# Kernel optimization log

Hardware: AMD Instinct MI355X
Metric: run time of the kernel (lower is better)

Reference implementation:

```python
import jax, jax.numpy as jnp
import numpy as np

N_GROUPS = 32
N_HEADS = 16
EPS = 1e-5


def group_norm(x, w, b):
    # x: [B, C, T]
    B, C, T = x.shape
    xg = x.reshape(B, N_GROUPS, C // N_GROUPS, T)
    mu = xg.mean(axis=(2, 3), keepdims=True)
    var = xg.var(axis=(2, 3), keepdims=True)
    xn = ((xg - mu) * jax.lax.rsqrt(var + EPS)).reshape(B, C, T)
    return xn * w[None, :, None] + b[None, :, None]


def setup_inputs() -> dict:
    key = jax.random.key(0)
    ks = jax.random.split(key, 5)
    B, C, T = 4, 1024, 1024
    return {
        "x": jax.random.normal(ks[0], (B, C, T), jnp.float32),
        "norm_weight": jnp.ones((C,), jnp.float32),
        "norm_bias": jnp.zeros((C,), jnp.float32),
        "qkv_w": jax.random.normal(ks[1], (3 * C, C), jnp.float32) * 0.02,
        "qkv_b": jax.random.normal(ks[2], (3 * C,), jnp.float32) * 0.02,
        "proj_w": jax.random.normal(ks[3], (C, C), jnp.float32) * 0.02,
        "proj_b": jax.random.normal(ks[4], (C,), jnp.float32) * 0.02,
    }


def reference(x, norm_weight, norm_bias, qkv_w, qkv_b, proj_w, proj_b):
    B, C, T = x.shape
    H = N_HEADS
    ch = C // H
    # GroupNorm + 1x1 conv to QKV: [B, 3C, T]
    xn = group_norm(x, norm_weight, norm_bias)
    qkv = jnp.einsum('oc,bct->bot', qkv_w, xn) + qkv_b[None, :, None]
    # Legacy layout: [B, H*3*ch, T] -> [B, H, 3, ch, T]
    qkv = qkv.reshape(B, H, 3, ch, T)
    q, k, v = qkv[:, :, 0], qkv[:, :, 1], qkv[:, :, 2]
    scale = 1.0 / jnp.sqrt(jnp.sqrt(jnp.asarray(ch, x.dtype)))
    w = jnp.einsum('bhct,bhcs->bhts', q * scale, k * scale)
    w = jax.nn.softmax(w.astype(jnp.float32), axis=-1).astype(w.dtype)
    a = jnp.einsum('bhts,bhcs->bhct', w, v).reshape(B, C, T)
    h = jnp.einsum('oc,bct->bot', proj_w, a) + proj_b[None, :, None]
    return x + h
```

## Files before the change

kernel.cpp:

```cpp
#include <hip/hip_runtime.h>
#include <hip/hip_bf16.h>

typedef __bf16 bf16;
typedef bf16  bf16x4 __attribute__((ext_vector_type(4)));
typedef bf16  bf16x8 __attribute__((ext_vector_type(8)));
typedef float f32x4  __attribute__((ext_vector_type(4)));

union B8 { bf16x8 v; bf16 e[8]; };
union B4 { bf16x4 v; bf16 e[4]; };
union F4 { f32x4 v; float e[4]; };

#define GLOAD_LDS16(g, l)                                            \
  __builtin_amdgcn_global_load_lds(                                  \
      (const __attribute__((address_space(1))) void*)(g),            \
      (__attribute__((address_space(3))) void*)(l), 16, 0, 0)

#define SWZ(arr, R, c8) (*(const bf16x8*)&(arr)[(size_t)(R) * 64 + (((c8) ^ ((R) & 7)) << 3)])

__global__ __launch_bounds__(256) void pre_kernel(
    const float* __restrict__ x, const float* __restrict__ w,
    const float* __restrict__ bias, bf16* __restrict__ xnt,
    const float* __restrict__ qkvw, const float* __restrict__ qkvb,
    const float* __restrict__ pw,
    bf16* __restrict__ Wb, bf16* __restrict__ Pb, float* __restrict__ bs)
{
  const int tid = threadIdx.x;

  if (blockIdx.x >= 128) {
    const int row = blockIdx.x - 128;
    if (row < 3072) {
      const float s = ((row % 192) < 128) ? 0.42468158f : 1.0f;
      const float4 a = ((const float4*)(qkvw + (size_t)row * 1024))[tid];
      B4 o;
      o.e[0] = (bf16)(a.x * s); o.e[1] = (bf16)(a.y * s);
      o.e[2] = (bf16)(a.z * s); o.e[3] = (bf16)(a.w * s);
      ((bf16x4*)(Wb + (size_t)row * 1024))[tid] = o.v;
      if (tid == 0) bs[row] = qkvb[row] * s;
    } else {
      const int r = row - 3072;
      const float4 a = ((const float4*)(pw + (size_t)r * 1024))[tid];
      B4 o;
      o.e[0] = (bf16)a.x; o.e[1] = (bf16)a.y;
      o.e[2] = (bf16)a.z; o.e[3] = (bf16)a.w;
      ((bf16x4*)(Pb + (size_t)r * 1024))[tid] = o.v;
    }
    return;
  }

  const int blk = blockIdx.x;
  const int b = blk >> 5, g = blk & 31;
  const float* xp = x + (size_t)(b * 1024 + g * 32) * 1024;

  float s = 0.f, ss = 0.f;
  for (int ch = tid; ch < 4096; ch += 256) {
    const float4* p = (const float4*)(xp + (size_t)ch * 8);
    float4 u0 = p[0], u1 = p[1];
    s  += u0.x + u0.y + u0.z + u0.w + u1.x + u1.y + u1.z + u1.w;
    ss += u0.x*u0.x + u0.y*u0.y + u0.z*u0.z + u0.w*u0.w
        + u1.x*u1.x + u1.y*u1.y + u1.z*u1.z + u1.w*u1.w;
  }
  #pragma unroll
  for (int m = 1; m < 64; m <<= 1) { s += __shfl_xor(s, m); ss += __shfl_xor(ss, m); }

  __shared__ float red[8];
  __shared__ float stats[2];
  const int wave = tid >> 6, lane = tid & 63;
  if (lane == 0) { red[wave] = s; red[4 + wave] = ss; }
  __syncthreads();
  if (tid == 0) {
    float ts  = red[0] + red[1] + red[2] + red[3];
    float tss = red[4] + red[5] + red[6] + red[7];
    float mu  = ts * (1.f / 32768.f);
    float var = tss * (1.f / 32768.f) - mu * mu;
    stats[0] = mu;
    stats[1] = rsqrtf(var + 1e-5f);
  }
  __syncthreads();
  const float mu = stats[0], rs = stats[1];

  for (int ti = 0; ti < 4; ++ti) {
    const int t = ti * 256 + tid;
    B8 o[4];
    #pragma unroll
    for (int cc = 0; cc < 32; ++cc) {
      const float wt = w[g * 32 + cc] * rs;
      const float bsv = bias[g * 32 + cc];
      const float v = xp[(size_t)cc * 1024 + t];
      o[cc >> 3].e[cc & 7] = (bf16)((v - mu) * wt + bsv);
    }
    bf16* dst = xnt + (size_t)(b * 1024 + t) * 1024 + g * 32;
    #pragma unroll
    for (int j = 0; j < 4; ++j) *(bf16x8*)(dst + j * 8) = o[j].v;
  }
}

__global__ __launch_bounds__(512, 2) void gemm_qkv_kernel(
    const bf16* __restrict__ xnt, const bf16* __restrict__ Wb,
    const float* __restrict__ bs, bf16* __restrict__ qkT, bf16* __restrict__ vv)
{
  const int bid = blockIdx.x;
  const int k = bid & 7, c = bid >> 3;
  const int bym = (k & 3) * 4 + (c & 3);
  const int bxn = (k >> 2) * 8 + (c >> 2);
  const int n0 = bxn * 192, m0 = bym * 256;
  const int head = bxn;

  __shared__ __align__(16) bf16 Al[2][256 * 64];
  __shared__ __align__(16) bf16 Bl[2][192 * 64];

  const int tid  = threadIdx.x;
  const int wave = tid >> 6, lane = tid & 63;
  const int quad = lane >> 4, l15 = lane & 15;
  const int wr = wave >> 2, wc = wave & 3;
  const int lrow = lane >> 3, lp = lane & 7;
  const int sc8 = (lp ^ lrow) << 3;

  #define STAGE(bufn, kt) do {                                                \
    _Pragma("unroll")                                                         \
    for (int cc = 0; cc < 4; ++cc)                                            \
      GLOAD_LDS16(xnt + (size_t)(m0 + cc * 64 + wave * 8 + lrow) * 1024 +     \
                      (size_t)(kt) * 64 + sc8,                                \
                  &Al[bufn][(cc * 64 + wave * 8) * 64]);                      \
    _Pragma("unroll")                                                         \
    for (int cc = 0; cc < 3; ++cc)                                            \
      GLOAD_LDS16(Wb + (size_t)(n0 + cc * 64 + wave * 8 + lrow) * 1024 +      \
                      (size_t)(kt) * 64 + sc8,                                \
                  &Bl[bufn][(cc * 64 + wave * 8) * 64]);                      \
  } while (0)

  F4 acc[8][3];
  #pragma unroll
  for (int i = 0; i < 8; ++i)
    #pragma unroll
    for (int j = 0; j < 3; ++j) acc[i][j].v = (f32x4){0.f, 0.f, 0.f, 0.f};

  STAGE(0, 0);
  __syncthreads();

  for (int t = 0; t < 16; ++t) {
    const int cb = t & 1;

    bf16x8 af[2][8], bfr[2][3];
    #pragma unroll
    for (int kk = 0; kk < 2; ++kk) {
      #pragma unroll
      for (int nt = 0; nt < 3; ++nt)
        bfr[kk][nt] = SWZ(Bl[cb], wc * 48 + nt * 16 + l15, kk * 4 + quad);
      #pragma unroll
      for (int mt = 0; mt < 8; ++mt)
        af[kk][mt] = SWZ(Al[cb], wr * 128 + mt * 16 + l15, kk * 4 + quad);
    }

    if (t + 1 < 16) STAGE(cb ^ 1, t + 1);

    #pragma unroll
    for (int kk = 0; kk < 2; ++kk)
      #pragma unroll
      for (int mt = 0; mt < 8; ++mt)
        #pragma unroll
        for (int nt = 0; nt < 3; ++nt)
          acc[mt][nt].v = __builtin_amdgcn_mfma_f32_16x16x32_bf16(
              af[kk][mt], bfr[kk][nt], acc[mt][nt].v, 0, 0, 0);

    __syncthreads();
  }
  #undef STAGE

  const int z  = m0 >> 10;
  const int tb = (m0 & 1023) + wr * 128;
  float bbv[3];
  #pragma unroll
  for (int nt = 0; nt < 3; ++nt) bbv[nt] = bs[n0 + wc * 48 + nt * 16 + l15];

  #pragma unroll
  for (int mt = 0; mt < 8; ++mt)
    #pragma unroll
    for (int r = 0; r < 4; ++r) {
      const int m = m0 + wr * 128 + mt * 16 + quad * 4 + r;
      #pragma unroll
      for (int nt = 0; nt < 3; ++nt) {
        const int r192 = wc * 48 + nt * 16;
        if (r192 < 128)
          qkT[(size_t)m * 2048 + head * 128 + r192 + l15] =
              (bf16)(acc[mt][nt].e[r] + bbv[nt]);
      }
    }
  #pragma unroll
  for (int nt = 0; nt < 3; ++nt) {
    const int r192 = wc * 48 + nt * 16;
    if (r192 >= 128) {
      bf16* vrow = vv + ((size_t)z * 1024 + head * 64 + (r192 - 128) + l15) * 1024;
      #pragma unroll
      for (int mt = 0; mt < 8; ++mt) {
        B4 pk;
        #pragma unroll
        for (int r = 0; r < 4; ++r) pk.e[r] = (bf16)(acc[mt][nt].e[r] + bbv[nt]);
        *(bf16x4*)&vrow[tb + mt * 16 + quad * 4] = pk.v;
      }
    }
  }
}

__global__ __launch_bounds__(512, 2) void gemm_proj_kernel(
    const bf16* __restrict__ Pb, const bf16* __restrict__ Bt,
    float* __restrict__ out, const float* __restrict__ bias,
    const float* __restrict__ resf)
{
  const int bid = blockIdx.x;
  const int swz = (bid & 7) * 32 + (bid >> 3);
  const int mp = swz & 7, np = swz >> 3;
  const int m0 = mp * 128;
  const int n0g = np * 128;

  __shared__ __align__(16) bf16 Al[2][2][128 * 64];
  __shared__ __align__(16) bf16 Bl[2][2][128 * 64];

  const int tid  = threadIdx.x;
  const int wave = tid >> 6, lane = tid & 63;
  const int quad = lane >> 4, l15 = lane & 15;
  const int wr = wave >> 2, wc = wave & 3;
  const int lrow = lane >> 3, lp = lane & 7;
  const int sc8 = (lp ^ lrow) << 3;

  #define STAGE(bufn, kt) do {                                                \
    _Pragma("unroll")                                                         \
    for (int h = 0; h < 2; ++h) {                                             \
      _Pragma("unroll")                                                       \
      for (int cc = 0; cc < 2; ++cc) {                                        \
        GLOAD_LDS16(Pb + (size_t)(m0 + cc * 64 + wave * 8 + lrow) * 1024 +    \
                        (size_t)(kt) * 128 + h * 64 + sc8,                    \
                    &Al[bufn][h][(cc * 64 + wave * 8) * 64]);                 \
        GLOAD_LDS16(Bt + (size_t)(n0g + cc * 64 + wave * 8 + lrow) * 1024 +   \
                        (size_t)(kt) * 128 + h * 64 + sc8,                    \
                    &Bl[bufn][h][(cc * 64 + wave * 8) * 64]);                 \
      }                                                                       \
    }                                                                         \
  } while (0)

  F4 acc[4][2];
  #pragma unroll
  for (int i = 0; i < 4; ++i)
    #pragma unroll
    for (int j = 0; j < 2; ++j) acc[i][j].v = (f32x4){0.f, 0.f, 0.f, 0.f};

  STAGE(0, 0);
  __syncthreads();

  for (int t = 0; t < 8; ++t) {
    const int cb = t & 1;

    bf16x8 af[2][2][4], bfr[2][2][2];
    #pragma unroll
    for (int h = 0; h < 2; ++h)
      #pragma unroll
      for (int kk = 0; kk < 2; ++kk) {
        #pragma unroll
        for (int mt = 0; mt < 4; ++mt)
          af[h][kk][mt] = SWZ(Al[cb][h], wr * 64 + mt * 16 + l15, kk * 4 + quad);
        #pragma unroll
        for (int nt = 0; nt < 2; ++nt)
          bfr[h][kk][nt] = SWZ(Bl[cb][h], wc * 32 + nt * 16 + l15, kk * 4 + quad);
      }

    if (t + 1 < 8) STAGE(cb ^ 1, t + 1);

    #pragma unroll
    for (int h = 0; h < 2; ++h)
      #pragma unroll
      for (int kk = 0; kk < 2; ++kk)
        #pragma unroll
        for (int mt = 0; mt < 4; ++mt)
          #pragma unroll
          for (int nt = 0; nt < 2; ++nt)
            acc[mt][nt].v = __builtin_amdgcn_mfma_f32_16x16x32_bf16(
                af[h][kk][mt], bfr[h][kk][nt], acc[mt][nt].v, 0, 0, 0);

    __syncthreads();
  }
  #undef STAGE

  const int z  = n0g >> 10;
  const int nl = n0g & 1023;
  const size_t zoff = (size_t)z * 1024 * 1024;
  #pragma unroll
  for (int mt = 0; mt < 4; ++mt) {
    #pragma unroll
    for (int r = 0; r < 4; ++r) {
      const int m = m0 + wr * 64 + mt * 16 + quad * 4 + r;
      const float bb = bias[m];
      #pragma unroll
      for (int nt = 0; nt < 2; ++nt) {
        const int n = nl + wc * 32 + nt * 16 + l15;
        out[zoff + (size_t)m * 1024 + n] =
            acc[mt][nt].e[r] + bb + resf[zoff + (size_t)m * 1024 + n];
      }
    }
  }
}

__global__ __launch_bounds__(512) void attn_kernel(
    const bf16* __restrict__ qkTin, const bf16* __restrict__ vmat,
    bf16* __restrict__ aout)
{
  const int h = blockIdx.x, tt = blockIdx.y, z = blockIdx.z;
  const bf16* qk = qkTin + (size_t)z * 1024 * 2048;
  const bf16* vp = vmat + (size_t)z * 1024 * 1024 + (size_t)(h * 64) * 1024;
  aout += (size_t)z * 1024 * 1024;
  const int t0 = tt * 256;

  __shared__ __align__(16) bf16 qP[256 * 64];
  __shared__ __align__(16) bf16 kl[2][64 * 64];
  __shared__ __align__(16) bf16 vl[2][64 * 64];

  const int tid  = threadIdx.x;
  const int wave = tid >> 6, lane = tid & 63;
  const int quad = lane >> 4, l15 = lane & 15;
  const int lrow = lane >> 3, lp = lane & 7;

  #pragma unroll
  for (int c = 0; c < 4; ++c) {
    const int row = wave * 32 + c * 8 + lrow;
    const int c8  = lp ^ (row & 7);
    GLOAD_LDS16(qk + (size_t)(t0 + row) * 2048 + h * 128 + c8 * 8,
                &qP[(wave * 32 + c * 8) * 64]);
  }
  const int r0 = wave * 8 + lrow;
  const int c80 = lp ^ (r0 & 7);
  GLOAD_LDS16(qk + (size_t)r0 * 2048 + h * 128 + 64 + c80 * 8, &kl[0][(wave * 8) * 64]);
  GLOAD_LDS16(vp + (size_t)r0 * 1024 + c80 * 8, &vl[0][(wave * 8) * 64]);
  __syncthreads();

  bf16x8 bq0[2], bq1[2];
  int prow[2];
  #pragma unroll
  for (int b = 0; b < 2; ++b) {
    const int Rq = wave * 32 + b * 16 + l15;
    bq0[b] = SWZ(qP, Rq, quad);
    bq1[b] = SWZ(qP, Rq, quad + 4);
    prow[b] = Rq;
  }

  float l_i[2] = {0.f, 0.f};
  F4 oacc[2][4];
  #pragma unroll
  for (int b = 0; b < 2; ++b)
    #pragma unroll
    for (int ct = 0; ct < 4; ++ct) oacc[b][ct].v = (f32x4){0.f, 0.f, 0.f, 0.f};

  const int pq8 = (quad & 1) * 4;

  int buf = 0;
  for (int s0 = 0; s0 < 1024; s0 += 64) {
    bf16x8 ak0[4], ak1[4], bv[2][4];
    #pragma unroll
    for (int st = 0; st < 4; ++st) {
      const int Rk = st * 16 + l15;
      ak0[st] = SWZ(kl[buf], Rk, quad);
      ak1[st] = SWZ(kl[buf], Rk, quad + 4);
    }
    #pragma unroll
    for (int ks = 0; ks < 2; ++ks)
      #pragma unroll
      for (int ct = 0; ct < 4; ++ct)
        bv[ks][ct] = SWZ(vl[buf], ct * 16 + l15, ks * 4 + quad);

    if (s0 + 64 < 1024) {
      const int nb = buf ^ 1, sn = s0 + 64;
      GLOAD_LDS16(qk + (size_t)(sn + r0) * 2048 + h * 128 + 64 + c80 * 8,
                  &kl[nb][(wave * 8) * 64]);
      GLOAD_LDS16(vp + (size_t)r0 * 1024 + sn + c80 * 8, &vl[nb][(wave * 8) * 64]);
    }

    #pragma unroll
    for (int b = 0; b < 2; ++b) {
      F4 sacc[4];
      #pragma unroll
      for (int st = 0; st < 4; ++st) sacc[st].v = (f32x4){0.f, 0.f, 0.f, 0.f};
      #pragma unroll
      for (int st = 0; st < 4; ++st) {
        sacc[st].v = __builtin_amdgcn_mfma_f32_16x16x32_bf16(ak0[st], bq0[b], sacc[st].v, 0, 0, 0);
        sacc[st].v = __builtin_amdgcn_mfma_f32_16x16x32_bf16(ak1[st], bq1[b], sacc[st].v, 0, 0, 0);
      }

      bf16* const pbase = &qP[(size_t)prow[b] * 64];
      #pragma unroll
      for (int st = 0; st < 4; ++st) {
        B4 pk;
        #pragma unroll
        for (int r = 0; r < 4; ++r) {
          const float p = __builtin_amdgcn_exp2f(sacc[st].e[r]);
          l_i[b] += p;
          pk.e[r] = (bf16)p;
        }
        const int c8 = (st * 2 + (quad >> 1)) ^ (prow[b] & 7);
        *(bf16x4*)(pbase + (c8 << 3) + pq8) = pk.v;
      }

      #pragma unroll
      for (int ks = 0; ks < 2; ++ks) {
        const bf16x8 ap = SWZ(qP, prow[b], ks * 4 + quad);
        #pragma unroll
        for (int ct = 0; ct < 4; ++ct)
          oacc[b][ct].v = __builtin_amdgcn_mfma_f32_16x16x32_bf16(
              ap, bv[ks][ct], oacc[b][ct].v, 0, 0, 0);
      }
    }
    __syncthreads();
    buf ^= 1;
  }

  #pragma unroll
  for (int b = 0; b < 2; ++b) {
    float li = l_i[b];
    li += __shfl_xor(li, 16);
    li += __shfl_xor(li, 32);
    const float inv = 1.f / li;
    float iv[4];
    #pragma unroll
    for (int r = 0; r < 4; ++r) iv[r] = __shfl(inv, quad * 4 + r);
    #pragma unroll
    for (int r = 0; r < 4; ++r) {
      const int t = t0 + wave * 32 + b * 16 + quad * 4 + r;
      #pragma unroll
      for (int ct = 0; ct < 4; ++ct)
        aout[(size_t)t * 1024 + h * 64 + ct * 16 + l15] = (bf16)(oacc[b][ct].e[r] * iv[r]);
    }
  }
}

extern "C" void kernel_launch(void* const* d_in, const int* in_sizes, int n_in,
                              void* d_out, int out_size, void* d_ws, size_t ws_size,
                              hipStream_t stream)
{
  const float* x    = (const float*)d_in[0];
  const float* nw   = (const float*)d_in[1];
  const float* nb   = (const float*)d_in[2];
  const float* qkvw = (const float*)d_in[3];
  const float* qkvb = (const float*)d_in[4];
  const float* pw   = (const float*)d_in[5];
  const float* pb   = (const float*)d_in[6];
  float* out = (float*)d_out;

  const long M1 = 1024L * 1024L;
  bf16*  xnt = (bf16*)d_ws;
  bf16*  qkT = xnt + 4 * M1;
  bf16*  vv  = xnt + 12 * M1;
  bf16*  at  = xnt + 16 * M1;
  bf16*  Wb  = xnt + 20 * M1;
  bf16*  Pb  = xnt + 23 * M1;
  float* bs  = (float*)(xnt + 24 * M1);

  pre_kernel<<<dim3(4224), dim3(256), 0, stream>>>(x, nw, nb, xnt,
                                                   qkvw, qkvb, pw, Wb, Pb, bs);
  gemm_qkv_kernel<<<dim3(256), dim3(512), 0, stream>>>(xnt, Wb, bs, qkT, vv);
  attn_kernel<<<dim3(16, 4, 4), dim3(512), 0, stream>>>(qkT, vv, at);
  gemm_proj_kernel<<<dim3(256), dim3(512), 0, stream>>>(Pb, at, out, pb, x);
}
```

Measured before the change: 167.7 us.

## Triple-buffer A tiles in QKV GEMM with vmcnt-based partial waits

The QKV GEMM now keeps three LDS buffers for the activation tile and two for the weight tile. Activation tiles are prefetched two k-steps ahead. The full __syncthreads is replaced by s_waitcnt vmcnt(4) plus a barrier, so the newest A load can still be in flight while the next iteration runs. This aims to hide global-to-LDS latency better, at the cost of about 147KB of LDS per block and hand-tuned wait counts that depend on load issue order.

```diff
diff --git a/kernel.cpp b/kernel.cpp
--- a/kernel.cpp
+++ b/kernel.cpp
@@ -105,7 +105,7 @@
   const int n0 = bxn * 192, m0 = bym * 256;
   const int head = bxn;
 
-  __shared__ __align__(16) bf16 Al[2][256 * 64];
+  __shared__ __align__(16) bf16 Al[3][256 * 64];
   __shared__ __align__(16) bf16 Bl[2][192 * 64];
 
   const int tid  = threadIdx.x;
@@ -115,12 +115,14 @@
   const int lrow = lane >> 3, lp = lane & 7;
   const int sc8 = (lp ^ lrow) << 3;
 
-  #define STAGE(bufn, kt) do {                                                \
+  #define STAGE_A(bufn, kt) do {                                              \
     _Pragma("unroll")                                                         \
     for (int cc = 0; cc < 4; ++cc)                                            \
       GLOAD_LDS16(xnt + (size_t)(m0 + cc * 64 + wave * 8 + lrow) * 1024 +     \
                       (size_t)(kt) * 64 + sc8,                                \
                   &Al[bufn][(cc * 64 + wave * 8) * 64]);                      \
+  } while (0)
+  #define STAGE_B(bufn, kt) do {                                              \
     _Pragma("unroll")                                                         \
     for (int cc = 0; cc < 3; ++cc)                                            \
       GLOAD_LDS16(Wb + (size_t)(n0 + cc * 64 + wave * 8 + lrow) * 1024 +      \
@@ -134,24 +136,30 @@
     #pragma unroll
     for (int j = 0; j < 3; ++j) acc[i][j].v = (f32x4){0.f, 0.f, 0.f, 0.f};
 
-  STAGE(0, 0);
-  __syncthreads();
-
+  STAGE_B(0, 0);
+  STAGE_A(0, 0);
+  STAGE_A(1, 1);
+  asm volatile("s_waitcnt vmcnt(4)" ::: "memory");
+  __builtin_amdgcn_s_barrier();
+  asm volatile("" ::: "memory");
+
+  int ab = 0;
   for (int t = 0; t < 16; ++t) {
-    const int cb = t & 1;
+    const int bb = t & 1;
 
     bf16x8 af[2][8], bfr[2][3];
     #pragma unroll
     for (int kk = 0; kk < 2; ++kk) {
       #pragma unroll
       for (int nt = 0; nt < 3; ++nt)
-        bfr[kk][nt] = SWZ(Bl[cb], wc * 48 + nt * 16 + l15, kk * 4 + quad);
+        bfr[kk][nt] = SWZ(Bl[bb], wc * 48 + nt * 16 + l15, kk * 4 + quad);
       #pragma unroll
       for (int mt = 0; mt < 8; ++mt)
-        af[kk][mt] = SWZ(Al[cb], wr * 128 + mt * 16 + l15, kk * 4 + quad);
-    }
-
-    if (t + 1 < 16) STAGE(cb ^ 1, t + 1);
+        af[kk][mt] = SWZ(Al[ab], wr * 128 + mt * 16 + l15, kk * 4 + quad);
+    }
+
+    if (t + 1 < 16) STAGE_B((t + 1) & 1, t + 1);
+    if (t + 2 < 16) STAGE_A(ab == 0 ? 2 : ab - 1, t + 2);
 
     #pragma unroll
     for (int kk = 0; kk < 2; ++kk)
@@ -162,9 +170,19 @@
           acc[mt][nt].v = __builtin_amdgcn_mfma_f32_16x16x32_bf16(
               af[kk][mt], bfr[kk][nt], acc[mt][nt].v, 0, 0, 0);
 
-    __syncthreads();
-  }
-  #undef STAGE
+    if (t < 14) {
+      asm volatile("s_waitcnt vmcnt(4)" ::: "memory");
+      __builtin_amdgcn_s_barrier();
+      asm volatile("" ::: "memory");
+    } else if (t == 14) {
+      asm volatile("s_waitcnt vmcnt(0)" ::: "memory");
+      __builtin_amdgcn_s_barrier();
+      asm volatile("" ::: "memory");
+    }
+    ab = (ab == 2) ? 0 : ab + 1;
+  }
+  #undef STAGE_A
+  #undef STAGE_B
 
   const int z  = m0 >> 10;
   const int tb = (m0 & 1023) + wr * 128;
```

Measured after the change: 169.3 us. About the same (+1.0%).
